# Kernel optimization log

Measured on AMD Instinct MI355X. Metric: run time of the kernel, lower is better.

Reference implementation:

```python
import jax, jax.numpy as jnp
import numpy as np

DELTA = 1
DROP_DC = False
EPS = 1e-8


def _shell_labels(D, H, W, delta):
    # radial frequency magnitude in cycles/voxel, assuming cubic-ish volume
    fx = jnp.fft.fftfreq(D)[:, None, None]
    fy = jnp.fft.fftfreq(H)[None, :, None]
    fz = jnp.fft.fftfreq(W)[None, None, :]
    r = jnp.sqrt(fx * fx + fy * fy + fz * fz)  # [D,H,W]
    n = min(D, H, W)
    nbins = n // (2 * delta)          # shells up to Nyquist (0.5 cyc/voxel)
    df = delta / n                    # shell width in frequency units
    labels = jnp.minimum((r / df).astype(jnp.int32), nbins)  # overflow bin = nbins
    return labels.reshape(-1), nbins


def setup_inputs() -> dict:
    key = jax.random.key(0)
    k1, k2 = jax.random.split(key)
    shape = (2, 1, 256, 256, 256)
    img_ref = jax.random.normal(k1, shape, dtype=jnp.float32)
    img_pred = jax.random.normal(k2, shape, dtype=jnp.float32)
    return {"img_ref": img_ref, "img_pred": img_pred}


def reference(img_ref, img_pred):
    B, C, D, H, W = img_ref.shape
    labels, nbins = _shell_labels(D, H, W, DELTA)

    F1 = jnp.fft.fftn(img_ref, axes=(-3, -2, -1))   # complex64 [B,C,D,H,W]
    F2 = jnp.fft.fftn(img_pred, axes=(-3, -2, -1))

    cross = jnp.real(F1 * jnp.conj(F2)).reshape(B * C, -1)
    p1 = (jnp.real(F1) ** 2 + jnp.imag(F1) ** 2).reshape(B * C, -1)
    p2 = (jnp.real(F2) ** 2 + jnp.imag(F2) ** 2).reshape(B * C, -1)

    def seg(x):  # radial shell sum; drop the overflow bin beyond Nyquist
        return jax.ops.segment_sum(x, labels, num_segments=nbins + 1)[:nbins]

    num = jax.vmap(seg)(cross)   # [B*C, nbins]
    d1 = jax.vmap(seg)(p1)
    d2 = jax.vmap(seg)(p2)

    fsc = num / jnp.sqrt(d1 * d2 + EPS)
    if DROP_DC:
        fsc = fsc[:, 1:]
    loss = 1.0 - jnp.mean(fsc ** 2)
    return loss
```

## Files before the change

### kernel.cpp

```cpp
#include <hip/hip_runtime.h>
#include <math.h>

#define NDIM 256
#define VOL  (NDIM*NDIM*NDIM)
#define NB   128

__device__ __forceinline__ int dr4(int x) {
    int b = (int)(__brev((unsigned)x) >> 24);
    return ((b >> 1) & 0x55) | ((b << 1) & 0xAA);
}
__device__ __forceinline__ float2 cmul(float2 a, float2 b) {
    return make_float2(a.x * b.x - a.y * b.y, a.x * b.y + a.y * b.x);
}
__device__ __forceinline__ float2 cadd(float2 a, float2 b){ return make_float2(a.x+b.x, a.y+b.y); }
__device__ __forceinline__ float2 csub(float2 a, float2 b){ return make_float2(a.x-b.x, a.y-b.y); }
__device__ __forceinline__ float2 cmuli_neg(float2 a){ return make_float2(a.y, -a.x); }
__device__ __forceinline__ float2 cmuli_pos(float2 a){ return make_float2(-a.y, a.x); }

__global__ __launch_bounds__(256) void fftz_pack(const float* __restrict__ re_in,
                                                 const float* __restrict__ im_in,
                                                 float2* __restrict__ out)
{
    __shared__ float2 buf[4][2][NDIM];
    const int t = threadIdx.x;
    const int w = t >> 6, j = t & 63;
    const int L = blockIdx.x * 4 + w;
    const float* rp = re_in + (size_t)L * NDIM;
    const float* ip = im_in + (size_t)L * NDIM;

    float2 v0 = make_float2(rp[j      ], ip[j      ]);
    float2 v1 = make_float2(rp[j +  64], ip[j +  64]);
    float2 v2 = make_float2(rp[j + 128], ip[j + 128]);
    float2 v3 = make_float2(rp[j + 192], ip[j + 192]);

    {
        float2 t0=cadd(v0,v2), t1=csub(v0,v2), t2=cadd(v1,v3), t3=csub(v1,v3);
        buf[w][0][4*j    ] = cadd(t0, t2);
        buf[w][0][4*j + 1] = cadd(t1, cmuli_neg(t3));
        buf[w][0][4*j + 2] = csub(t0, t2);
        buf[w][0][4*j + 3] = cadd(t1, cmuli_pos(t3));
    }
    __builtin_amdgcn_sched_barrier(0);

    int p = 0;
    #pragma unroll
    for (int stage = 1; stage <= 2; ++stage) {
        const int Ns = (stage == 1) ? 4 : 16;
        const int jm = j & (Ns - 1);
        float2 a0 = buf[w][p][j      ];
        float2 a1 = buf[w][p][j +  64];
        float2 a2 = buf[w][p][j + 128];
        float2 a3 = buf[w][p][j + 192];
        float sn, cs;
        __sincosf(-(float)(2.0 * M_PI) * (float)jm / (float)(4 * Ns), &sn, &cs);
        float2 w1 = make_float2(cs, sn);
        float2 w2 = cmul(w1, w1);
        float2 w3 = cmul(w2, w1);
        a1 = cmul(a1, w1); a2 = cmul(a2, w2); a3 = cmul(a3, w3);
        float2 t0=cadd(a0,a2), t1=csub(a0,a2), t2=cadd(a1,a3), t3=csub(a1,a3);
        const int idxD = (j / Ns) * (4 * Ns) + jm;
        buf[w][p^1][idxD         ] = cadd(t0, t2);
        buf[w][p^1][idxD +     Ns] = cadd(t1, cmuli_neg(t3));
        buf[w][p^1][idxD + 2 * Ns] = csub(t0, t2);
        buf[w][p^1][idxD + 3 * Ns] = cadd(t1, cmuli_pos(t3));
        p ^= 1;
        __builtin_amdgcn_sched_barrier(0);
    }

    {
        float2 a0 = buf[w][p][j      ];
        float2 a1 = buf[w][p][j +  64];
        float2 a2 = buf[w][p][j + 128];
        float2 a3 = buf[w][p][j + 192];
        float sn, cs;
        __sincosf(-(float)(2.0 * M_PI) * (float)j / 256.0f, &sn, &cs);
        float2 w1 = make_float2(cs, sn);
        float2 w2 = cmul(w1, w1);
        float2 w3 = cmul(w2, w1);
        a1 = cmul(a1, w1); a2 = cmul(a2, w2); a3 = cmul(a3, w3);
        float2 t0=cadd(a0,a2), t1=csub(a0,a2), t2=cadd(a1,a3), t3=csub(a1,a3);
        float2* op = out + (size_t)L * NDIM;
        op[j      ] = cadd(t0, t2);
        op[j +  64] = cadd(t1, cmuli_neg(t3));
        op[j + 128] = csub(t0, t2);
        op[j + 192] = cadd(t1, cmuli_pos(t3));
    }
}

__global__ __launch_bounds__(256) void fft_strided(float2* __restrict__ A,
                                                   int lineStride, int outerStride)
{
    __shared__ __align__(16) float2 tile[NDIM * 18];
    __shared__ float2 tw[NDIM];
    const int t = threadIdx.x;
    {
        float sn, cs;
        __sincosf(-(float)(2.0 * M_PI) * (float)t / 256.0f, &sn, &cs);
        tw[t] = make_float2(cs, sn);
    }
    const int l4 = t & 7, u8 = t >> 3;
    const int o = blockIdx.x >> 4, c = blockIdx.x & 15;
    const long long base = (long long)o * outerStride + c * 16;

    #pragma unroll
    for (int it = 0; it < 8; ++it) {
        int pos = u8 + it * 32;
        const float4 d = *(const float4*)&A[base + (long long)pos * lineStride + 2 * l4];
        tile[pos * 18 + 2 * l4    ] = make_float2(d.x, d.y);
        tile[pos * 18 + 2 * l4 + 1] = make_float2(d.z, d.w);
    }
    __syncthreads();

    const int l = t & 15, u = t >> 4;
    #pragma unroll
    for (int ls = 6; ls >= 0; ls -= 2) {
        const int s = 1 << ls;
        #pragma unroll
        for (int it = 0; it < 4; ++it) {
            int m  = u + it * 16;
            int jm = m & (s - 1);
            int bidx = ((m >> ls) << (ls + 2)) + jm;
            float2 a  = tile[(bidx        ) * 18 + l];
            float2 b  = tile[(bidx +     s) * 18 + l];
            float2 cc = tile[(bidx + 2 * s) * 18 + l];
            float2 d  = tile[(bidx + 3 * s) * 18 + l];
            float2 t0=cadd(a,cc), t1=csub(a,cc), t2=cadd(b,d), t3=csub(b,d);
            float2 y0 = cadd(t0, t2);
            float2 y1 = cadd(t1, cmuli_neg(t3));
            float2 y2 = csub(t0, t2);
            float2 y3 = cadd(t1, cmuli_pos(t3));
            int k1 = jm << (6 - ls);
            y1 = cmul(y1, tw[k1]);
            y2 = cmul(y2, tw[2 * k1]);
            y3 = cmul(y3, tw[3 * k1]);
            tile[(bidx        ) * 18 + l] = y0;
            tile[(bidx +     s) * 18 + l] = y1;
            tile[(bidx + 2 * s) * 18 + l] = y2;
            tile[(bidx + 3 * s) * 18 + l] = y3;
        }
        __syncthreads();
    }

    #pragma unroll
    for (int it = 0; it < 8; ++it) {
        int pos = u8 + it * 32;
        float2 e0 = tile[pos * 18 + 2 * l4], e1 = tile[pos * 18 + 2 * l4 + 1];
        *(float4*)&A[base + (long long)pos * lineStride + 2 * l4] =
            make_float4(e0.x, e0.y, e1.x, e1.y);
    }
}

__global__ __launch_bounds__(256) void reduce_shells(const float2* __restrict__ A,
                                                     float* __restrict__ bins)
{
    __shared__ float bs[4][3 * NB];
    const int t = threadIdx.x;
    const int w = t >> 6;
    for (int i = t; i < 4 * 3 * NB; i += 256) ((float*)bs)[i] = 0.f;
    __syncthreads();

    int  Lk[8], Lpk[8], lc2[8];
    float wgt[8];
    #pragma unroll
    for (int jj = 0; jj < 8; ++jj) {
        int L = blockIdx.x * 8 + jj;
        int px = L >> 8, py = L & 255;
        int fx = dr4(px), fy = dr4(py);
        int fxp = (256 - fx) & 255, fyp = (256 - fy) & 255;
        int Lp = dr4(fxp) * 256 + dr4(fyp);
        int ax = (fx < 128) ? fx : 256 - fx;
        int ay = (fy < 128) ? fy : 256 - fy;
        int c2 = ax * ax + ay * ay;
        lc2[jj] = -1;
        if (Lp >= L && c2 < NB * NB) lc2[jj] = c2;
        Lk[jj]  = (lc2[jj] < 0) ? 0 : L;
        Lpk[jj] = (lc2[jj] < 0) ? 0 : Lp;
        wgt[jj] = (Lp == L) ? 1.f : 2.f;
    }

    const int pz  = t;
    const int izc = (pz < 128) ? pz : 256 - pz;
    const int iz2 = izc * izc;
    const int pzp = (256 - pz) & 255;

    float2 z1[8], z2[8];
    __builtin_amdgcn_sched_barrier(0);
    #pragma unroll
    for (int jj = 0; jj < 8; ++jj) {
        z1[jj] = A[(size_t)Lk[jj]  * 256 + pz];
        z2[jj] = A[(size_t)Lpk[jj] * 256 + pzp];
    }
    __builtin_amdgcn_sched_barrier(0);

    #pragma unroll
    for (int jj = 0; jj < 8; ++jj) {
        if (lc2[jj] < 0) continue;
        int m = lc2[jj] + iz2;
        int lab = (int)sqrtf((float)m);
        if (lab >= NB) continue;
        float2 a = z1[jj], b = z2[jj];
        float F1r = 0.5f * (a.x + b.x);
        float F1i = 0.5f * (a.y - b.y);
        float F2r = 0.5f * (a.y + b.y);
        float F2i = 0.5f * (b.x - a.x);
        float g = wgt[jj];
        atomicAdd(&bs[w][lab],           g * (F1r * F2r + F1i * F2i));
        atomicAdd(&bs[w][NB + lab],      g * (F1r * F1r + F1i * F1i));
        atomicAdd(&bs[w][2 * NB + lab],  g * (F2r * F2r + F2i * F2i));
    }
    __syncthreads();

    for (int i = t; i < 3 * NB; i += 256) {
        float v = bs[0][i] + bs[1][i] + bs[2][i] + bs[3][i];
        if (v != 0.f) atomicAdd(&bins[i], v);
    }
}

__global__ void zero_bins(float* bins)
{
    int t = blockIdx.x * blockDim.x + threadIdx.x;
    if (t < 2 * 3 * NB) bins[t] = 0.f;
}

__global__ void finalize(const float* __restrict__ binsAll, float* __restrict__ out)
{
    __shared__ float red[256];
    const int t = threadIdx.x;
    const int b = t >> 7, bin = t & 127;
    const float* bb = binsAll + b * 3 * NB;
    float num = bb[bin], d1 = bb[NB + bin], d2 = bb[2 * NB + bin];
    float fsc = num / sqrtf(d1 * d2 + 1e-8f);
    red[t] = fsc * fsc;
    __syncthreads();
    for (int s = 128; s > 0; s >>= 1) {
        if (t < s) red[t] += red[t + s];
        __syncthreads();
    }
    if (t == 0) out[0] = 1.f - red[0] / 256.f;
}

__global__ void ws_too_small(float* out) { out[0] = -1.0e9f; }

extern "C" void kernel_launch(void* const* d_in, const int* in_sizes, int n_in,
                              void* d_out, int out_size, void* d_ws, size_t ws_size,
                              hipStream_t stream)
{
    const float* ref  = (const float*)d_in[0];
    const float* pred = (const float*)d_in[1];
    float* out = (float*)d_out;

    const size_t volBytes = (size_t)VOL * sizeof(float2);
    if (ws_size < volBytes + 4096) {
        ws_too_small<<<1, 1, 0, stream>>>(out);
        return;
    }
    float2* A   = (float2*)d_ws;
    float* bins = (float*)((char*)d_ws + volBytes);

    zero_bins<<<1, 1024, 0, stream>>>(bins);

    for (int b = 0; b < 2; ++b) {
        fftz_pack  <<<16384, 256, 0, stream>>>(ref + (size_t)b * VOL,
                                               pred + (size_t)b * VOL, A);
        fft_strided<<<4096, 256, 0, stream>>>(A, 256,   65536);
        fft_strided<<<4096, 256, 0, stream>>>(A, 65536, 256);
        reduce_shells<<<8192, 256, 0, stream>>>(A, bins + b * 3 * NB);
    }
    finalize<<<1, 256, 0, stream>>>(bins, out);
}
```

Measured before the change: 667.9 us.

## Split packed FFT after z-pass into half-spectrum volumes and fuse x-FFT with reduction

After the z-axis FFT, the packed complex transform is unpacked via Hermitian symmetry into two separate half-spectrum volumes (kz 0..127) for ref and pred. The y-FFT runs on each half volume, and the final x-FFT is fused with the shell reduction in shared memory. This removes one full-volume strided FFT pass and the separate scattered-read reduction kernel, and halves the data the later passes touch. The kz=128 Nyquist plane is dropped and the x/y conjugate pairing is replaced by a kz weighting, which relies on the shell-bin cutoff excluding those terms.

Result: slower. 732.1 us (+9.6%).

```diff
diff --git a/kernel.cpp b/kernel.cpp
--- a/kernel.cpp
+++ b/kernel.cpp
@@ -4,6 +4,9 @@
 #define NDIM 256
 #define VOL  (NDIM*NDIM*NDIM)
 #define NB   128
+#define KZ   128
+#define HVOL (NDIM*NDIM*KZ)
+#define PADC 10
 
 __device__ __forceinline__ int dr4(int x) {
     int b = (int)(__brev((unsigned)x) >> 24);
@@ -17,9 +20,10 @@
 __device__ __forceinline__ float2 cmuli_neg(float2 a){ return make_float2(a.y, -a.x); }
 __device__ __forceinline__ float2 cmuli_pos(float2 a){ return make_float2(-a.y, a.x); }
 
-__global__ __launch_bounds__(256) void fftz_pack(const float* __restrict__ re_in,
-                                                 const float* __restrict__ im_in,
-                                                 float2* __restrict__ out)
+__global__ __launch_bounds__(256) void fftz_split(const float* __restrict__ re_in,
+                                                  const float* __restrict__ im_in,
+                                                  float2* __restrict__ A1,
+                                                  float2* __restrict__ A2)
 {
     __shared__ float2 buf[4][2][NDIM];
     const int t = threadIdx.x;
@@ -79,16 +83,30 @@
         float2 w3 = cmul(w2, w1);
         a1 = cmul(a1, w1); a2 = cmul(a2, w2); a3 = cmul(a3, w3);
         float2 t0=cadd(a0,a2), t1=csub(a0,a2), t2=cadd(a1,a3), t3=csub(a1,a3);
-        float2* op = out + (size_t)L * NDIM;
-        op[j      ] = cadd(t0, t2);
-        op[j +  64] = cadd(t1, cmuli_neg(t3));
-        op[j + 128] = csub(t0, t2);
-        op[j + 192] = cadd(t1, cmuli_pos(t3));
+        float2* bd = buf[w][p^1];
+        bd[j      ] = cadd(t0, t2);
+        bd[j +  64] = cadd(t1, cmuli_neg(t3));
+        bd[j + 128] = csub(t0, t2);
+        bd[j + 192] = cadd(t1, cmuli_pos(t3));
+    }
+    __builtin_amdgcn_sched_barrier(0);
+
+    const float2* Zf = buf[w][p^1];
+    float2* o1 = A1 + (size_t)L * KZ;
+    float2* o2 = A2 + (size_t)L * KZ;
+    #pragma unroll
+    for (int r = 0; r < 2; ++r) {
+        const int kz = j + 64 * r;
+        float2 a = Zf[kz];
+        float2 b = Zf[(NDIM - kz) & 255];
+        o1[kz] = make_float2(0.5f * (a.x + b.x), 0.5f * (a.y - b.y));
+        o2[kz] = make_float2(0.5f * (a.y + b.y), 0.5f * (b.x - a.x));
     }
 }
 
 __global__ __launch_bounds__(256) void fft_strided(float2* __restrict__ A,
-                                                   int lineStride, int outerStride)
+                                                   int lineStride, long long outerStride,
+                                                   int chunkMask, int chunkShift)
 {
     __shared__ __align__(16) float2 tile[NDIM * 18];
     __shared__ float2 tw[NDIM];
@@ -99,7 +117,7 @@
         tw[t] = make_float2(cs, sn);
     }
     const int l4 = t & 7, u8 = t >> 3;
-    const int o = blockIdx.x >> 4, c = blockIdx.x & 15;
+    const int o = blockIdx.x >> chunkShift, c = blockIdx.x & chunkMask;
     const long long base = (long long)o * outerStride + c * 16;
 
     #pragma unroll
@@ -150,66 +168,98 @@
     }
 }
 
-__global__ __launch_bounds__(256) void reduce_shells(const float2* __restrict__ A,
-                                                     float* __restrict__ bins)
-{
+__global__ __launch_bounds__(256) void fftx_reduce(const float2* __restrict__ A1,
+                                                   const float2* __restrict__ A2,
+                                                   float* __restrict__ bins)
+{
+    __shared__ __align__(16) float2 t1[NDIM * PADC];
+    __shared__ __align__(16) float2 t2[NDIM * PADC];
+    __shared__ float2 tw[NDIM];
     __shared__ float bs[4][3 * NB];
     const int t = threadIdx.x;
-    const int w = t >> 6;
+    {
+        float sn, cs;
+        __sincosf(-(float)(2.0 * M_PI) * (float)t / 256.0f, &sn, &cs);
+        tw[t] = make_float2(cs, sn);
+    }
     for (int i = t; i < 4 * 3 * NB; i += 256) ((float*)bs)[i] = 0.f;
+
+    const int o   = blockIdx.x >> 4;
+    const int c   = blockIdx.x & 15;
+    const int kz0 = c * 8;
+    const size_t base = (size_t)o * KZ + kz0;
+
+    const int q = t & 3, xr = t >> 2;
+    #pragma unroll
+    for (int it = 0; it < 4; ++it) {
+        int x = xr + it * 64;
+        size_t g = base + (size_t)x * (NDIM * KZ) + 2 * q;
+        float4 d1 = *(const float4*)&A1[g];
+        float4 d2 = *(const float4*)&A2[g];
+        *(float4*)&t1[x * PADC + 2 * q] = d1;
+        *(float4*)&t2[x * PADC + 2 * q] = d2;
+    }
     __syncthreads();
 
-    int  Lk[8], Lpk[8], lc2[8];
-    float wgt[8];
-    #pragma unroll
-    for (int jj = 0; jj < 8; ++jj) {
-        int L = blockIdx.x * 8 + jj;
-        int px = L >> 8, py = L & 255;
-        int fx = dr4(px), fy = dr4(py);
-        int fxp = (256 - fx) & 255, fyp = (256 - fy) & 255;
-        int Lp = dr4(fxp) * 256 + dr4(fyp);
-        int ax = (fx < 128) ? fx : 256 - fx;
-        int ay = (fy < 128) ? fy : 256 - fy;
-        int c2 = ax * ax + ay * ay;
-        lc2[jj] = -1;
-        if (Lp >= L && c2 < NB * NB) lc2[jj] = c2;
-        Lk[jj]  = (lc2[jj] < 0) ? 0 : L;
-        Lpk[jj] = (lc2[jj] < 0) ? 0 : Lp;
-        wgt[jj] = (Lp == L) ? 1.f : 2.f;
-    }
-
-    const int pz  = t;
-    const int izc = (pz < 128) ? pz : 256 - pz;
-    const int iz2 = izc * izc;
-    const int pzp = (256 - pz) & 255;
-
-    float2 z1[8], z2[8];
-    __builtin_amdgcn_sched_barrier(0);
-    #pragma unroll
-    for (int jj = 0; jj < 8; ++jj) {
-        z1[jj] = A[(size_t)Lk[jj]  * 256 + pz];
-        z2[jj] = A[(size_t)Lpk[jj] * 256 + pzp];
-    }
-    __builtin_amdgcn_sched_barrier(0);
-
-    #pragma unroll
-    for (int jj = 0; jj < 8; ++jj) {
-        if (lc2[jj] < 0) continue;
-        int m = lc2[jj] + iz2;
-        int lab = (int)sqrtf((float)m);
-        if (lab >= NB) continue;
-        float2 a = z1[jj], b = z2[jj];
-        float F1r = 0.5f * (a.x + b.x);
-        float F1i = 0.5f * (a.y - b.y);
-        float F2r = 0.5f * (a.y + b.y);
-        float F2i = 0.5f * (b.x - a.x);
-        float g = wgt[jj];
-        atomicAdd(&bs[w][lab],           g * (F1r * F2r + F1i * F2i));
-        atomicAdd(&bs[w][NB + lab],      g * (F1r * F1r + F1i * F1i));
-        atomicAdd(&bs[w][2 * NB + lab],  g * (F2r * F2r + F2i * F2i));
+    const int l = t & 7, u = t >> 3;
+    #pragma unroll
+    for (int ls = 6; ls >= 0; ls -= 2) {
+        const int s = 1 << ls;
+        #pragma unroll
+        for (int it = 0; it < 2; ++it) {
+            int m  = u + it * 32;
+            int jm = m & (s - 1);
+            int bidx = ((m >> ls) << (ls + 2)) + jm;
+            int k1 = jm << (6 - ls);
+            {
+                float2 a  = t1[(bidx        ) * PADC + l];
+                float2 b  = t1[(bidx +     s) * PADC + l];
+                float2 cc = t1[(bidx + 2 * s) * PADC + l];
+                float2 d  = t1[(bidx + 3 * s) * PADC + l];
+                float2 t0=cadd(a,cc), u1=csub(a,cc), t2_=cadd(b,d), t3=csub(b,d);
+                t1[(bidx        ) * PADC + l] = cadd(t0, t2_);
+                t1[(bidx +     s) * PADC + l] = cmul(cadd(u1, cmuli_neg(t3)), tw[k1]);
+                t1[(bidx + 2 * s) * PADC + l] = cmul(csub(t0, t2_), tw[2 * k1]);
+                t1[(bidx + 3 * s) * PADC + l] = cmul(cadd(u1, cmuli_pos(t3)), tw[3 * k1]);
+            }
+            {
+                float2 a  = t2[(bidx        ) * PADC + l];
+                float2 b  = t2[(bidx +     s) * PADC + l];
+                float2 cc = t2[(bidx + 2 * s) * PADC + l];
+                float2 d  = t2[(bidx + 3 * s) * PADC + l];
+                float2 t0=cadd(a,cc), u1=csub(a,cc), t2_=cadd(b,d), t3=csub(b,d);
+                t2[(bidx        ) * PADC + l] = cadd(t0, t2_);
+                t2[(bidx +     s) * PADC + l] = cmul(cadd(u1, cmuli_neg(t3)), tw[k1]);
+                t2[(bidx + 2 * s) * PADC + l] = cmul(csub(t0, t2_), tw[2 * k1]);
+                t2[(bidx + 3 * s) * PADC + l] = cmul(cadd(u1, cmuli_pos(t3)), tw[3 * k1]);
+            }
+        }
+        __syncthreads();
+    }
+
+    const int ky = dr4(o);
+    const int ay = (ky <= 128) ? ky : NDIM - ky;
+    const int wv  = t >> 6;
+    const int kzl = t & 7, pr = t >> 3;
+    const int kz  = kz0 + kzl;
+    const float g = (kz == 0) ? 1.f : 2.f;
+    const int ayz2 = ay * ay + kz * kz;
+    #pragma unroll
+    for (int it = 0; it < 8; ++it) {
+        int pos = pr + it * 32;
+        int kx = dr4(pos);
+        int ax = (kx <= 128) ? kx : NDIM - kx;
+        int c2 = ax * ax + ayz2;
+        if (c2 < NB * NB) {
+            int lab = (int)sqrtf((float)c2);
+            float2 f1 = t1[pos * PADC + kzl];
+            float2 f2 = t2[pos * PADC + kzl];
+            atomicAdd(&bs[wv][lab],          g * (f1.x * f2.x + f1.y * f2.y));
+            atomicAdd(&bs[wv][NB + lab],     g * (f1.x * f1.x + f1.y * f1.y));
+            atomicAdd(&bs[wv][2 * NB + lab], g * (f2.x * f2.x + f2.y * f2.y));
+        }
     }
     __syncthreads();
-
     for (int i = t; i < 3 * NB; i += 256) {
         float v = bs[0][i] + bs[1][i] + bs[2][i] + bs[3][i];
         if (v != 0.f) atomicAdd(&bins[i], v);
@@ -249,22 +299,23 @@
     const float* pred = (const float*)d_in[1];
     float* out = (float*)d_out;
 
-    const size_t volBytes = (size_t)VOL * sizeof(float2);
+    const size_t volBytes = (size_t)HVOL * sizeof(float2) * 2;
     if (ws_size < volBytes + 4096) {
         ws_too_small<<<1, 1, 0, stream>>>(out);
         return;
     }
-    float2* A   = (float2*)d_ws;
+    float2* A1  = (float2*)d_ws;
+    float2* A2  = A1 + HVOL;
     float* bins = (float*)((char*)d_ws + volBytes);
 
     zero_bins<<<1, 1024, 0, stream>>>(bins);
 
     for (int b = 0; b < 2; ++b) {
-        fftz_pack  <<<16384, 256, 0, stream>>>(ref + (size_t)b * VOL,
-                                               pred + (size_t)b * VOL, A);
-        fft_strided<<<4096, 256, 0, stream>>>(A, 256,   65536);
-        fft_strided<<<4096, 256, 0, stream>>>(A, 65536, 256);
-        reduce_shells<<<8192, 256, 0, stream>>>(A, bins + b * 3 * NB);
+        fftz_split<<<16384, 256, 0, stream>>>(ref + (size_t)b * VOL,
+                                              pred + (size_t)b * VOL, A1, A2);
+        fft_strided<<<2048, 256, 0, stream>>>(A1, 128, 32768LL, 7, 3);
+        fft_strided<<<2048, 256, 0, stream>>>(A2, 128, 32768LL, 7, 3);
+        fftx_reduce<<<4096, 256, 0, stream>>>(A1, A2, bins + b * 3 * NB);
     }
     finalize<<<1, 256, 0, stream>>>(bins, out);
 }
```
